# Optimization experiments

Measured on AMD Instinct MI355X. Metric: run time of the kernel, lower is better.

Reference implementation:

```python
import jax, jax.numpy as jnp
import numpy as np

N = 50000        # node_num
E = 1600000      # num edges
F_IN = 8
HID = 1000
R = 100          # robustness_length


def setup_inputs() -> dict:
    key = jax.random.key(0)
    ks = jax.random.split(key, 16)
    X = jax.random.normal(ks[0], (N, F_IN), dtype=jnp.float32)
    edge_index = jax.random.randint(ks[1], (2, E), 0, N, dtype=jnp.int64)
    s = 1.0 / np.sqrt(F_IN)
    # SAGEConv mean-aggr params (PyG: out = lin_l(aggr) + lin_r(x), lin_r has no bias)
    lin_l_w = jax.random.uniform(ks[2], (1, F_IN), jnp.float32, -s, s)
    lin_l_b = jax.random.uniform(ks[3], (1,), jnp.float32, -s, s)
    lin_r_w = jax.random.uniform(ks[4], (1, F_IN), jnp.float32, -s, s)
    # SAGEConv max-aggr params
    lin_l1_w = jax.random.uniform(ks[5], (1, F_IN), jnp.float32, -s, s)
    lin_l1_b = jax.random.uniform(ks[6], (1,), jnp.float32, -s, s)
    lin_r1_w = jax.random.uniform(ks[7], (1, F_IN), jnp.float32, -s, s)
    # MLP params
    s0 = 1.0 / np.sqrt(N)
    W0 = jax.random.uniform(ks[8], (HID, N), jnp.float32, -s0, s0)
    b0 = jax.random.uniform(ks[9], (HID,), jnp.float32, -s0, s0)
    s1 = 1.0 / np.sqrt(HID)
    W1 = jax.random.uniform(ks[10], (HID, HID), jnp.float32, -s1, s1)
    b1 = jax.random.uniform(ks[11], (HID,), jnp.float32, -s1, s1)
    W2 = jax.random.uniform(ks[12], (R, HID), jnp.float32, -s1, s1)
    b2 = jax.random.uniform(ks[13], (R,), jnp.float32, -s1, s1)
    return dict(X=X, edge_index=edge_index,
                lin_l_w=lin_l_w, lin_l_b=lin_l_b, lin_r_w=lin_r_w,
                lin_l1_w=lin_l1_w, lin_l1_b=lin_l1_b, lin_r1_w=lin_r1_w,
                W0=W0, b0=b0, W1=W1, b1=b1, W2=W2, b2=b2)


def reference(X, edge_index, lin_l_w, lin_l_b, lin_r_w,
              lin_l1_w, lin_l1_b, lin_r1_w,
              W0, b0, W1, b1, W2, b2):
    src, dst = edge_index[0], edge_index[1]
    msgs = X[src]  # [E, F_IN] gathered neighbor features
    cnt = jax.ops.segment_sum(jnp.ones((E,), jnp.float32), dst, num_segments=N)
    # mean aggregation (empty -> 0)
    agg_mean = jax.ops.segment_sum(msgs, dst, num_segments=N) / jnp.maximum(cnt, 1.0)[:, None]
    # max aggregation (empty -> 0, per PyG scatter-max fill)
    agg_max = jax.ops.segment_max(msgs, dst, num_segments=N)
    agg_max = jnp.where(cnt[:, None] > 0, agg_max, 0.0)
    # SAGEConv: lin_l(aggr) + lin_r(x)
    h_mean = jax.nn.relu(agg_mean @ lin_l_w.T + lin_l_b + X @ lin_r_w.T)   # [N,1]
    h_max = jax.nn.relu(agg_max @ lin_l1_w.T + lin_l1_b + X @ lin_r1_w.T)  # [N,1]
    x = (h_mean + h_max).reshape(-1)  # [N]
    X_embedding = x
    h = jax.nn.relu(W0 @ x + b0)
    h = jax.nn.relu(W1 @ h + b1)
    out = jax.nn.relu(W2 @ h + b2)
    return (X_embedding, out)
```

## Files before the change

### kernel.cpp

```cpp
#include <hip/hip_runtime.h>

#define N_NODES 50000
#define N_EDGES 1600000
#define F_IN 8
#define HID 1000
#define R_OUT 100

#define BSHIFT 6
#define NPB 64
#define NB 782
#define CAP_B 2432
#define CHUNK 4096
#define NBIN_BLOCKS ((N_EDGES + CHUNK - 1) / CHUNK)
#define NCHUNK0 25


__device__ __forceinline__ unsigned fkey(float f) {
    unsigned b = __float_as_uint(f);
    return (b & 0x80000000u) ? ~b : (b | 0x80000000u);
}
__device__ __forceinline__ float funkey(unsigned k) {
    unsigned b = (k & 0x80000000u) ? (k & 0x7fffffffu) : ~k;
    return __uint_as_float(b);
}

__global__ void init_kernel(unsigned* __restrict__ p, int nzero,
                            const float* __restrict__ b0, float* __restrict__ h0) {
    int i = blockIdx.x * blockDim.x + threadIdx.x;
    if (i < nzero) p[i] = 0u;
    if (i < HID) h0[i] = b0[i];
}

__global__ void bin_kernel(const int* __restrict__ ei,
                           const float* __restrict__ X,
                           const float* __restrict__ wl,
                           int* __restrict__ cursor,
                           unsigned* __restrict__ binned,
                           int* __restrict__ ovf_cnt,
                           float* __restrict__ ovf_sum,
                           unsigned* __restrict__ ovf_max) {
    __shared__ unsigned sEntry[CHUNK];
    __shared__ unsigned short sBucket[CHUNK];
    __shared__ int hist[NB];
    __shared__ int pos[NB];
    __shared__ int base[NB];
    int tid = threadIdx.x;
    int e0 = blockIdx.x * CHUNK;
    int e1 = e0 + CHUNK;
    if (e1 > N_EDGES) e1 = N_EDGES;
    int ne = e1 - e0;

    for (int i = tid; i < NB; i += 256) { hist[i] = 0; pos[i] = 0; }
    __syncthreads();

    const int4* s4 = (const int4*)(ei + e0);
    const int4* d4 = (const int4*)(ei + N_EDGES + e0);
    int n4 = ne >> 2;
    for (int j4 = tid; j4 < n4; j4 += 256) {
        int4 s = s4[j4];
        int4 d = d4[j4];
        int jj = j4 << 2;
        int sv[4] = {s.x, s.y, s.z, s.w};
        int dv[4] = {d.x, d.y, d.z, d.w};
#pragma unroll
        for (int m = 0; m < 4; ++m) {
            int b = dv[m] >> BSHIFT;
            sEntry[jj + m] = (unsigned)sv[m] | ((unsigned)(dv[m] & (NPB - 1)) << 16);
            sBucket[jj + m] = (unsigned short)b;
            atomicAdd(&hist[b], 1);
        }
    }
    __syncthreads();

    for (int b = tid; b < NB; b += 256) {
        int h = hist[b];
        base[b] = (h > 0) ? atomicAdd(&cursor[b], h) : 0;
    }
    __syncthreads();

    for (int j = tid; j < ne; j += 256) {
        unsigned entry = sEntry[j];
        int b = sBucket[j];
        int p = atomicAdd(&pos[b], 1);
        int gp = base[b] + p;
        if (gp < CAP_B) {
            binned[(size_t)b * CAP_B + gp] = entry;
        } else {
            int src = entry & 0xFFFF;
            int dst = b * NPB + (int)(entry >> 16);
            const float4* X4 = (const float4*)(X + src * F_IN);
            float4 a = X4[0], bb = X4[1];
            float f[8] = {a.x, a.y, a.z, a.w, bb.x, bb.y, bb.z, bb.w};
            float dacc = 0.f;
#pragma unroll
            for (int k = 0; k < 8; ++k) dacc += f[k] * wl[k];
            atomicAdd(&ovf_cnt[dst], 1);
            atomicAdd(&ovf_sum[dst], dacc);
            unsigned* mb = ovf_max + (size_t)dst * 8;
#pragma unroll
            for (int k = 0; k < 8; ++k) atomicMax(&mb[k], fkey(f[k]));
        }
    }
}

__global__ void agg_kernel(const int* __restrict__ cursor,
                           const unsigned* __restrict__ binned,
                           const int* __restrict__ ovf_cnt,
                           const float* __restrict__ ovf_sum,
                           const unsigned* __restrict__ ovf_max,
                           const float* __restrict__ X,
                           const float* __restrict__ lin_l_w,
                           const float* __restrict__ lin_l_b,
                           const float* __restrict__ lin_r_w,
                           const float* __restrict__ lin_l1_w,
                           const float* __restrict__ lin_l1_b,
                           const float* __restrict__ lin_r1_w,
                           float* __restrict__ xemb) {
    __shared__ float sSum[NPB];
    __shared__ int   sCnt[NPB];
    __shared__ unsigned sMax[8][NPB];

    int b = blockIdx.x;
    int tid = threadIdx.x;
    int n = cursor[b];
    if (n > CAP_B) n = CAP_B;

    if (tid < NPB) { sSum[tid] = 0.f; sCnt[tid] = 0; }
    for (int i = tid; i < 8 * NPB; i += 256) ((unsigned*)sMax)[i] = 0u;
    __syncthreads();

    float wl[8];
#pragma unroll
    for (int k = 0; k < 8; ++k) wl[k] = lin_l_w[k];

    const unsigned* blist = binned + (size_t)b * CAP_B;
    for (int j = tid; j < n; j += 256) {
        unsigned e = blist[j];
        int src = e & 0xFFFF;
        int d = e >> 16;
        const float4* X4 = (const float4*)(X + src * F_IN);
        float4 a = X4[0], c = X4[1];
        float f[8] = {a.x, a.y, a.z, a.w, c.x, c.y, c.z, c.w};
        float dot = 0.f;
#pragma unroll
        for (int k = 0; k < 8; ++k) dot += f[k] * wl[k];
        atomicAdd(&sSum[d], dot);
        atomicAdd(&sCnt[d], 1);
#pragma unroll
        for (int k = 0; k < 8; ++k) atomicMax(&sMax[k][d], fkey(f[k]));
    }
    __syncthreads();

    if (tid < NPB) {
        int node = b * NPB + tid;
        if (node < N_NODES) {
            int oc = ovf_cnt[node];
            int total = sCnt[tid] + oc;
            float sd = sSum[tid] + ovf_sum[node];
            unsigned km[8];
#pragma unroll
            for (int k = 0; k < 8; ++k) km[k] = sMax[k][tid];
            if (oc > 0) {
                const unsigned* mb = ovf_max + (size_t)node * 8;
#pragma unroll
                for (int k = 0; k < 8; ++k) km[k] = (km[k] > mb[k]) ? km[k] : mb[k];
            }
            float c = (float)total;
            float mean_dot = sd / fmaxf(c, 1.0f);
            const float4* X4 = (const float4*)(X + node * F_IN);
            float4 a = X4[0], bb = X4[1];
            float f[8] = {a.x, a.y, a.z, a.w, bb.x, bb.y, bb.z, bb.w};
            float dr = 0.f, dr1 = 0.f, dmax = 0.f;
            bool nonempty = (total > 0);
#pragma unroll
            for (int k = 0; k < 8; ++k) {
                float m = nonempty ? funkey(km[k]) : 0.0f;
                dmax += m * lin_l1_w[k];
                dr   += f[k] * lin_r_w[k];
                dr1  += f[k] * lin_r1_w[k];
            }
            float hm = fmaxf(mean_dot + lin_l_b[0] + dr, 0.f);
            float hx = fmaxf(dmax + lin_l1_b[0] + dr1, 0.f);
            xemb[node] = hm + hx;
        }
    }
}


template <int BLOCK, int NCHUNK>
__global__ void gemv_accum(const float* __restrict__ W,
                           const float* __restrict__ x,
                           float* __restrict__ y, int cols) {
    int c = blockIdx.x;
    int row = blockIdx.y;
    int chunk = cols / NCHUNK;
    const float4* W4 = (const float4*)(W + (size_t)row * cols + (size_t)c * chunk);
    const float4* x4 = (const float4*)(x + c * chunk);
    int n4 = chunk >> 2;
    float s = 0.f;
    for (int j = threadIdx.x; j < n4; j += BLOCK) {
        float4 w = W4[j], xx = x4[j];
        s += w.x * xx.x + w.y * xx.y + w.z * xx.z + w.w * xx.w;
    }
#pragma unroll
    for (int off = 32; off > 0; off >>= 1) s += __shfl_down(s, off, 64);
    __shared__ float red[BLOCK / 64];
    int t = threadIdx.x;
    if ((t & 63) == 0) red[t >> 6] = s;
    __syncthreads();
    if (t == 0) {
        float tot = 0.f;
#pragma unroll
        for (int w = 0; w < BLOCK / 64; ++w) tot += red[w];
        atomicAdd(&y[row], tot);
    }
}

template <int BLOCK, bool RELUX>
__global__ void gemv_relu(const float* __restrict__ W,
                          const float* __restrict__ x,
                          const float* __restrict__ bias,
                          float* __restrict__ y, int cols) {
    int row = blockIdx.x;
    const float4* W4 = (const float4*)(W + (size_t)row * cols);
    const float4* x4 = (const float4*)x;
    int n4 = cols >> 2;
    float s = 0.f;
    for (int j = threadIdx.x; j < n4; j += BLOCK) {
        float4 w = W4[j], xx = x4[j];
        if (RELUX) {
            xx.x = fmaxf(xx.x, 0.f); xx.y = fmaxf(xx.y, 0.f);
            xx.z = fmaxf(xx.z, 0.f); xx.w = fmaxf(xx.w, 0.f);
        }
        s += w.x * xx.x + w.y * xx.y + w.z * xx.z + w.w * xx.w;
    }
#pragma unroll
    for (int off = 32; off > 0; off >>= 1) s += __shfl_down(s, off, 64);
    __shared__ float red[BLOCK / 64];
    int t = threadIdx.x;
    if ((t & 63) == 0) red[t >> 6] = s;
    __syncthreads();
    if (t == 0) {
        float tot = 0.f;
#pragma unroll
        for (int w = 0; w < BLOCK / 64; ++w) tot += red[w];
        y[row] = fmaxf(tot + bias[row], 0.f);
    }
}


__global__ void init_ws_fb(unsigned* __restrict__ p, int n) {
    int i = blockIdx.x * blockDim.x + threadIdx.x;
    if (i < n) p[i] = 0u;
}

__global__ void edge_kernel_fb(const int* __restrict__ ei,
                               const float* __restrict__ X,
                               const float* __restrict__ wl,
                               float* __restrict__ sumw,
                               float* __restrict__ cnt,
                               unsigned* __restrict__ maxb) {
    int e = blockIdx.x * blockDim.x + threadIdx.x;
    if (e >= N_EDGES) return;
    int src = ei[e];
    int dst = ei[N_EDGES + e];
    const float4* X4 = (const float4*)(X + src * F_IN);
    float4 a = X4[0], b = X4[1];
    float f[8] = {a.x, a.y, a.z, a.w, b.x, b.y, b.z, b.w};
    float d = 0.f;
#pragma unroll
    for (int k = 0; k < 8; ++k) d += f[k] * wl[k];
    atomicAdd(&sumw[dst], d);
    atomicAdd(&cnt[dst], 1.0f);
    unsigned* mb = maxb + (size_t)dst * 8;
#pragma unroll
    for (int k = 0; k < 8; ++k) atomicMax(&mb[k], fkey(f[k]));
}

__global__ void node_kernel_fb(const float* __restrict__ X,
                               const float* __restrict__ sumw,
                               const float* __restrict__ cnt,
                               const unsigned* __restrict__ maxb,
                               const float* __restrict__ lin_l_b,
                               const float* __restrict__ lin_r_w,
                               const float* __restrict__ lin_l1_w,
                               const float* __restrict__ lin_l1_b,
                               const float* __restrict__ lin_r1_w,
                               float* __restrict__ xout) {
    int i = blockIdx.x * blockDim.x + threadIdx.x;
    if (i >= N_NODES) return;
    float c = cnt[i];
    float mean_dot = sumw[i] / fmaxf(c, 1.0f);
    const float4* X4 = (const float4*)(X + i * F_IN);
    float4 a = X4[0], b = X4[1];
    float f[8] = {a.x, a.y, a.z, a.w, b.x, b.y, b.z, b.w};
    const uint4* M4 = (const uint4*)(maxb + (size_t)i * 8);
    uint4 m0 = M4[0], m1 = M4[1];
    unsigned mk[8] = {m0.x, m0.y, m0.z, m0.w, m1.x, m1.y, m1.z, m1.w};
    float dr = 0.f, dr1 = 0.f, dmax = 0.f;
    bool nonempty = (c > 0.f);
#pragma unroll
    for (int k = 0; k < 8; ++k) {
        float mxv = nonempty ? funkey(mk[k]) : 0.0f;
        dmax += mxv * lin_l1_w[k];
        dr   += f[k] * lin_r_w[k];
        dr1  += f[k] * lin_r1_w[k];
    }
    float hm = fmaxf(mean_dot + lin_l_b[0] + dr, 0.f);
    float hx = fmaxf(dmax + lin_l1_b[0] + dr1, 0.f);
    xout[i] = hm + hx;
}


extern "C" void kernel_launch(void* const* d_in, const int* in_sizes, int n_in,
                              void* d_out, int out_size, void* d_ws, size_t ws_size,
                              hipStream_t stream) {
    const float* X        = (const float*)d_in[0];
    const int*   ei       = (const int*)d_in[1];
    const float* lin_l_w  = (const float*)d_in[2];
    const float* lin_l_b  = (const float*)d_in[3];
    const float* lin_r_w  = (const float*)d_in[4];
    const float* lin_l1_w = (const float*)d_in[5];
    const float* lin_l1_b = (const float*)d_in[6];
    const float* lin_r1_w = (const float*)d_in[7];
    const float* W0       = (const float*)d_in[8];
    const float* b0       = (const float*)d_in[9];
    const float* W1       = (const float*)d_in[10];
    const float* b1       = (const float*)d_in[11];
    const float* W2       = (const float*)d_in[12];
    const float* b2       = (const float*)d_in[13];

    float* xemb = (float*)d_out;
    float* out2 = xemb + N_NODES;

    const size_t zero_words = (size_t)NB + (size_t)N_NODES * 10;
    const size_t need_words = zero_words + (size_t)NB * CAP_B + 2 * HID;
    if (ws_size >= need_words * 4) {
        int*      cursor  = (int*)d_ws;
        int*      ovf_cnt = cursor + NB;
        float*    ovf_sum = (float*)(ovf_cnt + N_NODES);
        unsigned* ovf_max = (unsigned*)(ovf_sum + N_NODES);
        unsigned* binned  = ovf_max + (size_t)N_NODES * 8;
        float*    h0      = (float*)(binned + (size_t)NB * CAP_B);
        float*    h1      = h0 + HID;

        hipLaunchKernelGGL(init_kernel, dim3(((int)zero_words + 255) / 256), dim3(256), 0, stream,
                           (unsigned*)d_ws, (int)zero_words, b0, h0);
        hipLaunchKernelGGL(bin_kernel, dim3(NBIN_BLOCKS), dim3(256), 0, stream,
                           ei, X, lin_l_w, cursor, binned, ovf_cnt, ovf_sum, ovf_max);
        hipLaunchKernelGGL(agg_kernel, dim3(NB), dim3(256), 0, stream,
                           cursor, binned, ovf_cnt, ovf_sum, ovf_max, X,
                           lin_l_w, lin_l_b, lin_r_w, lin_l1_w, lin_l1_b, lin_r1_w, xemb);

        hipLaunchKernelGGL((gemv_accum<256, NCHUNK0>), dim3(NCHUNK0, HID), dim3(256), 0, stream,
                           W0, xemb, h0, N_NODES);
        hipLaunchKernelGGL((gemv_relu<256, true>), dim3(HID), dim3(256), 0, stream,
                           W1, h0, b1, h1, HID);
        hipLaunchKernelGGL((gemv_relu<256, false>), dim3(R_OUT), dim3(256), 0, stream,
                           W2, h1, b2, out2, HID);
    } else {
        float*    sumw = (float*)d_ws;
        float*    cntf = sumw + N_NODES;
        unsigned* maxb = (unsigned*)(cntf + N_NODES);
        float*    h0   = (float*)(maxb + (size_t)N_NODES * 8);
        float*    h1   = h0 + HID;

        int zw = N_NODES * 10;
        hipLaunchKernelGGL(init_ws_fb, dim3((zw + 255) / 256), dim3(256), 0, stream,
                           (unsigned*)d_ws, zw);
        hipLaunchKernelGGL(edge_kernel_fb, dim3((N_EDGES + 255) / 256), dim3(256), 0, stream,
                           ei, X, lin_l_w, sumw, cntf, maxb);
        hipLaunchKernelGGL(node_kernel_fb, dim3((N_NODES + 255) / 256), dim3(256), 0, stream,
                           X, sumw, cntf, maxb, lin_l_b, lin_r_w, lin_l1_w, lin_l1_b,
                           lin_r1_w, xemb);
        hipLaunchKernelGGL((gemv_relu<256, false>), dim3(HID), dim3(256), 0, stream,
                           W0, xemb, b0, h0, N_NODES);
        hipLaunchKernelGGL((gemv_relu<256, false>), dim3(HID), dim3(256), 0, stream,
                           W1, h0, b1, h1, HID);
        hipLaunchKernelGGL((gemv_relu<256, false>), dim3(R_OUT), dim3(256), 0, stream,
                           W2, h1, b2, out2, HID);
    }
}
```

Baseline: 357.1 us.

## Fuse all six stages into one cooperative persistent kernel with grid syncs

Replaces the six separate launches (init, edge binning, aggregation, and three GEMVs) with a single cooperative kernel of 768 persistent blocks. The stages are separated by grid.sync, and each GEMV stage now does one row-chunk per wavefront with atomic accumulation. This removes per-launch overhead and the idle gaps between kernels. In exchange it adds grid-wide barrier costs, lower occupancy from the fixed grid and launch bounds, and smaller binning chunks, which mean more global cursor atomics. If the cooperative launch fails, the old multi-kernel path runs instead.

Measured after the change: 836.8 us. 2.34x slower.

```diff
diff --git a/kernel.cpp b/kernel.cpp
--- a/kernel.cpp
+++ b/kernel.cpp
@@ -1,4 +1,7 @@
 #include <hip/hip_runtime.h>
+#include <hip/hip_cooperative_groups.h>
+
+namespace cg = cooperative_groups;
 
 #define N_NODES 50000
 #define N_EDGES 1600000
@@ -10,9 +13,15 @@
 #define NPB 64
 #define NB 782
 #define CAP_B 2432
+#define NCHUNK0 25
+#define COLS0 (N_NODES / NCHUNK0)
+
+#define GRID_F 768
+#define CHUNK_F 2048
+#define NCHUNKS_BIN ((N_EDGES + CHUNK_F - 1) / CHUNK_F)
+
 #define CHUNK 4096
 #define NBIN_BLOCKS ((N_EDGES + CHUNK - 1) / CHUNK)
-#define NCHUNK0 25
 
 
 __device__ __forceinline__ unsigned fkey(float f) {
@@ -23,6 +32,258 @@
     unsigned b = (k & 0x80000000u) ? (k & 0x7fffffffu) : ~k;
     return __uint_as_float(b);
 }
+
+
+struct FusedArgs {
+    const float* X;
+    const int*   ei;
+    const float* lin_l_w;
+    const float* lin_l_b;
+    const float* lin_r_w;
+    const float* lin_l1_w;
+    const float* lin_l1_b;
+    const float* lin_r1_w;
+    const float* W0;
+    const float* b0;
+    const float* W1;
+    const float* b1;
+    const float* W2;
+    const float* b2;
+    int*      cursor;
+    unsigned* binned;
+    int*      ovf_cnt;
+    float*    ovf_sum;
+    unsigned* ovf_max;
+    float*    h0;
+    float*    h1;
+    float*    xemb;
+    float*    out2;
+    int       zero_words;
+};
+
+__global__ __launch_bounds__(256, 3) void fused_kernel(FusedArgs A) {
+    cg::grid_group grid = cg::this_grid();
+
+    __shared__ union {
+        struct {
+            unsigned entry[CHUNK_F];
+            unsigned short bucket[CHUNK_F];
+            int hist[NB];
+            int pos[NB];
+            int base[NB];
+        } p1;
+        struct {
+            float sum[NPB];
+            int   cnt[NPB];
+            unsigned mx[8][NPB];
+        } p2;
+    } sm;
+
+    const int tid  = threadIdx.x;
+    const int bid  = blockIdx.x;
+    const int nblk = gridDim.x;
+    const int gtid = bid * 256 + tid;
+    const int nthr = nblk * 256;
+
+    {
+        unsigned* zb = (unsigned*)A.cursor;
+        for (int i = gtid; i < A.zero_words; i += nthr) zb[i] = 0u;
+        for (int i = gtid; i < HID; i += nthr) A.h0[i] = A.b0[i];
+    }
+    grid.sync();
+
+    for (int chunk = bid; chunk < NCHUNKS_BIN; chunk += nblk) {
+        int e0 = chunk * CHUNK_F;
+        int e1 = e0 + CHUNK_F;
+        if (e1 > N_EDGES) e1 = N_EDGES;
+        int ne = e1 - e0;
+
+        for (int i = tid; i < NB; i += 256) { sm.p1.hist[i] = 0; sm.p1.pos[i] = 0; }
+        __syncthreads();
+
+        const int4* s4 = (const int4*)(A.ei + e0);
+        const int4* d4 = (const int4*)(A.ei + N_EDGES + e0);
+        int n4 = ne >> 2;
+        for (int j4 = tid; j4 < n4; j4 += 256) {
+            int4 s = s4[j4];
+            int4 d = d4[j4];
+            int jj = j4 << 2;
+            int sv[4] = {s.x, s.y, s.z, s.w};
+            int dv[4] = {d.x, d.y, d.z, d.w};
+#pragma unroll
+            for (int m = 0; m < 4; ++m) {
+                int b = dv[m] >> BSHIFT;
+                sm.p1.entry[jj + m] = (unsigned)sv[m] | ((unsigned)(dv[m] & (NPB - 1)) << 16);
+                sm.p1.bucket[jj + m] = (unsigned short)b;
+                atomicAdd(&sm.p1.hist[b], 1);
+            }
+        }
+        __syncthreads();
+
+        for (int b = tid; b < NB; b += 256) {
+            int h = sm.p1.hist[b];
+            sm.p1.base[b] = (h > 0) ? atomicAdd(&A.cursor[b], h) : 0;
+        }
+        __syncthreads();
+
+        for (int j = tid; j < ne; j += 256) {
+            unsigned entry = sm.p1.entry[j];
+            int b = sm.p1.bucket[j];
+            int p = atomicAdd(&sm.p1.pos[b], 1);
+            int gp = sm.p1.base[b] + p;
+            if (gp < CAP_B) {
+                A.binned[(size_t)b * CAP_B + gp] = entry;
+            } else {
+                int src = entry & 0xFFFF;
+                int dst = b * NPB + (int)(entry >> 16);
+                const float4* X4 = (const float4*)(A.X + src * F_IN);
+                float4 a = X4[0], bb = X4[1];
+                float f[8] = {a.x, a.y, a.z, a.w, bb.x, bb.y, bb.z, bb.w};
+                float dacc = 0.f;
+#pragma unroll
+                for (int k = 0; k < 8; ++k) dacc += f[k] * A.lin_l_w[k];
+                atomicAdd(&A.ovf_cnt[dst], 1);
+                atomicAdd(&A.ovf_sum[dst], dacc);
+                unsigned* mb = A.ovf_max + (size_t)dst * 8;
+#pragma unroll
+                for (int k = 0; k < 8; ++k) atomicMax(&mb[k], fkey(f[k]));
+            }
+        }
+        __syncthreads();
+    }
+    grid.sync();
+
+    {
+        float wl[8];
+#pragma unroll
+        for (int k = 0; k < 8; ++k) wl[k] = A.lin_l_w[k];
+
+        for (int b = bid; b < NB; b += nblk) {
+            int n = A.cursor[b];
+            if (n > CAP_B) n = CAP_B;
+
+            if (tid < NPB) { sm.p2.sum[tid] = 0.f; sm.p2.cnt[tid] = 0; }
+            for (int i = tid; i < 8 * NPB; i += 256) ((unsigned*)sm.p2.mx)[i] = 0u;
+            __syncthreads();
+
+            const unsigned* blist = A.binned + (size_t)b * CAP_B;
+            for (int j = tid; j < n; j += 256) {
+                unsigned e = blist[j];
+                int src = e & 0xFFFF;
+                int d = e >> 16;
+                const float4* X4 = (const float4*)(A.X + src * F_IN);
+                float4 a = X4[0], c = X4[1];
+                float f[8] = {a.x, a.y, a.z, a.w, c.x, c.y, c.z, c.w};
+                float dot = 0.f;
+#pragma unroll
+                for (int k = 0; k < 8; ++k) dot += f[k] * wl[k];
+                atomicAdd(&sm.p2.sum[d], dot);
+                atomicAdd(&sm.p2.cnt[d], 1);
+#pragma unroll
+                for (int k = 0; k < 8; ++k) atomicMax(&sm.p2.mx[k][d], fkey(f[k]));
+            }
+            __syncthreads();
+
+            if (tid < NPB) {
+                int node = b * NPB + tid;
+                if (node < N_NODES) {
+                    int oc = A.ovf_cnt[node];
+                    int total = sm.p2.cnt[tid] + oc;
+                    float sd = sm.p2.sum[tid] + A.ovf_sum[node];
+                    unsigned km[8];
+#pragma unroll
+                    for (int k = 0; k < 8; ++k) km[k] = sm.p2.mx[k][tid];
+                    if (oc > 0) {
+                        const unsigned* mb = A.ovf_max + (size_t)node * 8;
+#pragma unroll
+                        for (int k = 0; k < 8; ++k) km[k] = (km[k] > mb[k]) ? km[k] : mb[k];
+                    }
+                    float c = (float)total;
+                    float mean_dot = sd / fmaxf(c, 1.0f);
+                    const float4* X4 = (const float4*)(A.X + node * F_IN);
+                    float4 a = X4[0], bb = X4[1];
+                    float f[8] = {a.x, a.y, a.z, a.w, bb.x, bb.y, bb.z, bb.w};
+                    float dr = 0.f, dr1 = 0.f, dmax = 0.f;
+                    bool nonempty = (total > 0);
+#pragma unroll
+                    for (int k = 0; k < 8; ++k) {
+                        float m = nonempty ? funkey(km[k]) : 0.0f;
+                        dmax += m * A.lin_l1_w[k];
+                        dr   += f[k] * A.lin_r_w[k];
+                        dr1  += f[k] * A.lin_r1_w[k];
+                    }
+                    float hm = fmaxf(mean_dot + A.lin_l_b[0] + dr, 0.f);
+                    float hx = fmaxf(dmax + A.lin_l1_b[0] + dr1, 0.f);
+                    A.xemb[node] = hm + hx;
+                }
+            }
+            __syncthreads();
+        }
+    }
+    grid.sync();
+
+    {
+        int wid  = gtid >> 6;
+        int lane = gtid & 63;
+        int nw   = nthr >> 6;
+        for (int t = wid; t < NCHUNK0 * HID; t += nw) {
+            int c   = t % NCHUNK0;
+            int row = t / NCHUNK0;
+            const float4* W4 = (const float4*)(A.W0 + (size_t)row * N_NODES + (size_t)c * COLS0);
+            const float4* x4 = (const float4*)(A.xemb + c * COLS0);
+            float s = 0.f;
+#pragma unroll 2
+            for (int j = lane; j < (COLS0 >> 2); j += 64) {
+                float4 w = W4[j], xx = x4[j];
+                s += w.x * xx.x + w.y * xx.y + w.z * xx.z + w.w * xx.w;
+            }
+#pragma unroll
+            for (int off = 32; off > 0; off >>= 1) s += __shfl_down(s, off, 64);
+            if (lane == 0) atomicAdd(&A.h0[row], s);
+        }
+    }
+    grid.sync();
+
+    {
+        int wid  = gtid >> 6;
+        int lane = gtid & 63;
+        int nw   = nthr >> 6;
+        for (int row = wid; row < HID; row += nw) {
+            const float4* W4 = (const float4*)(A.W1 + (size_t)row * HID);
+            const float4* x4 = (const float4*)A.h0;
+            float s = 0.f;
+            for (int j = lane; j < (HID >> 2); j += 64) {
+                float4 w = W4[j], xx = x4[j];
+                xx.x = fmaxf(xx.x, 0.f); xx.y = fmaxf(xx.y, 0.f);
+                xx.z = fmaxf(xx.z, 0.f); xx.w = fmaxf(xx.w, 0.f);
+                s += w.x * xx.x + w.y * xx.y + w.z * xx.z + w.w * xx.w;
+            }
+#pragma unroll
+            for (int off = 32; off > 0; off >>= 1) s += __shfl_down(s, off, 64);
+            if (lane == 0) A.h1[row] = fmaxf(s + A.b1[row], 0.f);
+        }
+    }
+    grid.sync();
+
+    {
+        int wid  = gtid >> 6;
+        int lane = gtid & 63;
+        int nw   = nthr >> 6;
+        for (int row = wid; row < R_OUT; row += nw) {
+            const float4* W4 = (const float4*)(A.W2 + (size_t)row * HID);
+            const float4* x4 = (const float4*)A.h1;
+            float s = 0.f;
+            for (int j = lane; j < (HID >> 2); j += 64) {
+                float4 w = W4[j], xx = x4[j];
+                s += w.x * xx.x + w.y * xx.y + w.z * xx.z + w.w * xx.w;
+            }
+#pragma unroll
+            for (int off = 32; off > 0; off >>= 1) s += __shfl_down(s, off, 64);
+            if (lane == 0) A.out2[row] = fmaxf(s + A.b2[row], 0.f);
+        }
+    }
+}
+
 
 __global__ void init_kernel(unsigned* __restrict__ p, int nzero,
                             const float* __restrict__ b0, float* __restrict__ h0) {
@@ -186,7 +447,6 @@
     }
 }
 
-
 template <int BLOCK, int NCHUNK>
 __global__ void gemv_accum(const float* __restrict__ W,
                            const float* __restrict__ x,
@@ -247,7 +507,6 @@
         y[row] = fmaxf(tot + bias[row], 0.f);
     }
 }
-
 
 __global__ void init_ws_fb(unsigned* __restrict__ p, int n) {
     int i = blockIdx.x * blockDim.x + threadIdx.x;
@@ -344,20 +603,34 @@
         float*    h0      = (float*)(binned + (size_t)NB * CAP_B);
         float*    h1      = h0 + HID;
 
-        hipLaunchKernelGGL(init_kernel, dim3(((int)zero_words + 255) / 256), dim3(256), 0, stream,
-                           (unsigned*)d_ws, (int)zero_words, b0, h0);
-        hipLaunchKernelGGL(bin_kernel, dim3(NBIN_BLOCKS), dim3(256), 0, stream,
-                           ei, X, lin_l_w, cursor, binned, ovf_cnt, ovf_sum, ovf_max);
-        hipLaunchKernelGGL(agg_kernel, dim3(NB), dim3(256), 0, stream,
-                           cursor, binned, ovf_cnt, ovf_sum, ovf_max, X,
-                           lin_l_w, lin_l_b, lin_r_w, lin_l1_w, lin_l1_b, lin_r1_w, xemb);
-
-        hipLaunchKernelGGL((gemv_accum<256, NCHUNK0>), dim3(NCHUNK0, HID), dim3(256), 0, stream,
-                           W0, xemb, h0, N_NODES);
-        hipLaunchKernelGGL((gemv_relu<256, true>), dim3(HID), dim3(256), 0, stream,
-                           W1, h0, b1, h1, HID);
-        hipLaunchKernelGGL((gemv_relu<256, false>), dim3(R_OUT), dim3(256), 0, stream,
-                           W2, h1, b2, out2, HID);
+        FusedArgs fa;
+        fa.X = X; fa.ei = ei;
+        fa.lin_l_w = lin_l_w; fa.lin_l_b = lin_l_b; fa.lin_r_w = lin_r_w;
+        fa.lin_l1_w = lin_l1_w; fa.lin_l1_b = lin_l1_b; fa.lin_r1_w = lin_r1_w;
+        fa.W0 = W0; fa.b0 = b0; fa.W1 = W1; fa.b1 = b1; fa.W2 = W2; fa.b2 = b2;
+        fa.cursor = cursor; fa.binned = binned;
+        fa.ovf_cnt = ovf_cnt; fa.ovf_sum = ovf_sum; fa.ovf_max = ovf_max;
+        fa.h0 = h0; fa.h1 = h1; fa.xemb = xemb; fa.out2 = out2;
+        fa.zero_words = (int)zero_words;
+
+        void* kp[] = {(void*)&fa};
+        hipError_t err = hipLaunchCooperativeKernel((const void*)fused_kernel,
+                                                    dim3(GRID_F), dim3(256), kp, 0, stream);
+        if (err != hipSuccess) {
+            hipLaunchKernelGGL(init_kernel, dim3(((int)zero_words + 255) / 256), dim3(256), 0, stream,
+                               (unsigned*)d_ws, (int)zero_words, b0, h0);
+            hipLaunchKernelGGL(bin_kernel, dim3(NBIN_BLOCKS), dim3(256), 0, stream,
+                               ei, X, lin_l_w, cursor, binned, ovf_cnt, ovf_sum, ovf_max);
+            hipLaunchKernelGGL(agg_kernel, dim3(NB), dim3(256), 0, stream,
+                               cursor, binned, ovf_cnt, ovf_sum, ovf_max, X,
+                               lin_l_w, lin_l_b, lin_r_w, lin_l1_w, lin_l1_b, lin_r1_w, xemb);
+            hipLaunchKernelGGL((gemv_accum<256, NCHUNK0>), dim3(NCHUNK0, HID), dim3(256), 0, stream,
+                               W0, xemb, h0, N_NODES);
+            hipLaunchKernelGGL((gemv_relu<256, true>), dim3(HID), dim3(256), 0, stream,
+                               W1, h0, b1, h1, HID);
+            hipLaunchKernelGGL((gemv_relu<256, false>), dim3(R_OUT), dim3(256), 0, stream,
+                               W2, h1, b2, out2, HID);
+        }
     } else {
         float*    sumw = (float*)d_ws;
         float*    cntf = sumw + N_NODES;
```
